# Kernel tuning notes

Measured on AMD Instinct MI355X. Metric: run time of the kernel, lower is better.

Reference implementation:

```python
import jax, jax.numpy as jnp
import numpy as np

BATCH, N_GRAPHS, N_NODES, UNITS = 512, 3, 4096, 256

def setup_inputs() -> dict:
    key = jax.random.key(0)
    ks = jax.random.split(key, 11)
    return {
        "inputs": jax.random.normal(ks[0], (BATCH, N_NODES), jnp.float32),
        "state": jax.random.normal(ks[1], (BATCH, UNITS), jnp.float32),
        "adj": jax.random.uniform(ks[2], (N_GRAPHS, N_NODES, N_NODES), jnp.float32),
        "wa": jax.random.uniform(ks[3], (N_GRAPHS,), jnp.float32),
        "w_gcn": jax.random.normal(ks[4], (N_NODES, UNITS), jnp.float32) * (1.0 / np.sqrt(N_NODES)),
        "wz": jax.random.normal(ks[5], (UNITS, UNITS), jnp.float32) * 0.05,
        "uz": jax.random.normal(ks[6], (UNITS, UNITS), jnp.float32) * 0.05,
        "bz": jax.random.normal(ks[7], (UNITS,), jnp.float32) * 0.05,
        "wh": jax.random.normal(ks[8], (UNITS, UNITS), jnp.float32) * 0.05,
        "uh": jax.random.normal(ks[9], (UNITS, UNITS), jnp.float32) * 0.05,
        "bh": jax.random.normal(ks[10], (UNITS,), jnp.float32) * 0.05,
    }

def reference(inputs, state, adj, wa, w_gcn, wz, uz, bz, wh, uh, bh):
    # Weighted sum of the n_graphs adjacency matrices: [g],[g,n,n] -> [n,n]
    adj_mix = jnp.einsum('g,gnm->nm', wa, adj)
    # Graph conv: (inputs @ adj_mix) @ w_gcn, then ReLU -> [batch, units]
    x = jax.nn.relu(jnp.matmul(jnp.matmul(inputs, adj_mix), w_gcn))
    # GRU-style gating
    z = jax.nn.sigmoid(x @ wz + state @ uz + bz)
    h_tilde = jnp.tanh(x @ wh + state @ uh + bh)
    out = (1.0 - z) * state + z * h_tilde
    return out
```

## Files before the change

kernel.cpp:

```cpp
#include <hip/hip_runtime.h>
#include <stdint.h>

typedef _Float16 f16;
typedef __attribute__((ext_vector_type(8))) _Float16 f16x8;
typedef __attribute__((ext_vector_type(4))) float f32x4;

#define NN 4096
#define UN 256

__device__ __forceinline__ f16x8 ld_f16x8(const f16* p){ return *(const f16x8*)p; }
__device__ __forceinline__ f32x4 zero4(){ f32x4 z = {0.f,0.f,0.f,0.f}; return z; }


__global__ __launch_bounds__(256) void k0_prep(
    const float* __restrict__ wg, const float* __restrict__ wz,
    const float* __restrict__ uz, const float* __restrict__ wh,
    const float* __restrict__ uh,
    f16* __restrict__ wgB,
    f16* __restrict__ czB_h, f16* __restrict__ czB_l,
    f16* __restrict__ chB_h, f16* __restrict__ chB_l)
{
  __shared__ float lsA[32*256];
  __shared__ float lsB[32*256];
  const int t = threadIdx.x;
  const int b = blockIdx.x;
  if (b < 128){
    const int kcg = b;
    #pragma unroll 8
    for (int i = 0; i < 32; i++)
      lsA[i*256 + t] = wg[(size_t)(kcg*32 + i) * UN + t];
    __syncthreads();
    #pragma unroll
    for (int i = 0; i < 4; i++){
      int o = i*256 + t;
      int l = o & 63;
      int n = ((o >> 6) << 4) + (l & 15);
      int kl = (l >> 4) * 8;
      f16 v8[8];
      #pragma unroll
      for (int j = 0; j < 8; j++) v8[j] = (f16)lsA[(kl + j)*256 + n];
      *(uint4*)(wgB + ((size_t)kcg*1024 + o)*8) = *(const uint4*)v8;
    }
  } else {
    const int kcg = b - 128;
    #pragma unroll 8
    for (int i = 0; i < 32; i++){
      int kg = kcg*32 + i;
      lsA[i*256 + t] = (kg < 256) ? wz[(size_t)kg * UN + t]
                                  : uz[(size_t)(kg - 256) * UN + t];
      lsB[i*256 + t] = (kg < 256) ? wh[(size_t)kg * UN + t]
                                  : uh[(size_t)(kg - 256) * UN + t];
    }
    __syncthreads();
    #pragma unroll
    for (int i = 0; i < 4; i++){
      int o = i*256 + t;
      int l = o & 63;
      int n = ((o >> 6) << 4) + (l & 15);
      int kl = (l >> 4) * 8;
      f16 zh[8], zl[8], hh[8], hl[8];
      #pragma unroll
      for (int j = 0; j < 8; j++){
        float vz = lsA[(kl + j)*256 + n];
        float vh = lsB[(kl + j)*256 + n];
        f16 a = (f16)vz; zh[j] = a; zl[j] = (f16)(vz - (float)a);
        f16 c = (f16)vh; hh[j] = c; hl[j] = (f16)(vh - (float)c);
      }
      size_t off = ((size_t)kcg*1024 + o)*8;
      *(uint4*)(czB_h + off) = *(const uint4*)zh;
      *(uint4*)(czB_l + off) = *(const uint4*)zl;
      *(uint4*)(chB_h + off) = *(const uint4*)hh;
      *(uint4*)(chB_l + off) = *(const uint4*)hl;
    }
  }
}

__global__ __launch_bounds__(256) void k1_w2(
    const float* __restrict__ adj, const float* __restrict__ wa,
    const f16* __restrict__ wgB, float* __restrict__ W2p)
{
  const int t = threadIdx.x, lane = t & 63, wv = t >> 6;
  const int qm = lane & 15, quad = lane >> 4;
  const int mbase = blockIdx.x * 64 + wv * 16;
  const int kbase = blockIdx.y * 512;
  const float wa0 = wa[0], wa1 = wa[1], wa2 = wa[2];
  const size_t gs = (size_t)NN * NN;
  const float* pa = adj + (size_t)(mbase + qm) * NN + kbase + quad * 8;

  f32x4 acc[16];
  #pragma unroll
  for (int i = 0; i < 16; i++) acc[i] = zero4();

  f32x4 g[6];
  #pragma unroll
  for (int r = 0; r < 2; r++)
    #pragma unroll
    for (int gi = 0; gi < 3; gi++)
      g[gi*2 + r] = *(const f32x4*)(pa + (size_t)gi*gs + r*4);

  for (int step = 0; step < 16; step++){
    const int kc = step * 32;
    const int kcg = (kbase + kc) >> 5;
    const f16* pb = wgB + ((size_t)kcg*1024 + lane)*8;

    f16x8 bf[8];
    #pragma unroll
    for (int i = 0; i < 8; i++) bf[i] = ld_f16x8(pb + i*512);

    f16x8 ah, al;
    #pragma unroll
    for (int j = 0; j < 4; j++){
      float v0 = wa0*g[0][j] + wa1*g[2][j] + wa2*g[4][j];
      float v1 = wa0*g[1][j] + wa1*g[3][j] + wa2*g[5][j];
      f16 h0 = (f16)v0, h1 = (f16)v1;
      ah[j] = h0;   al[j] = (f16)(v0 - (float)h0);
      ah[4+j] = h1; al[4+j] = (f16)(v1 - (float)h1);
    }

    f32x4 gn[6];
    if (step < 15){
      const float* pan = pa + kc + 32;
      #pragma unroll
      for (int r = 0; r < 2; r++)
        #pragma unroll
        for (int gi = 0; gi < 3; gi++)
          gn[gi*2 + r] = *(const f32x4*)(pan + (size_t)gi*gs + r*4);
    }

    f16x8 bg[8];
    #pragma unroll
    for (int i = 0; i < 8; i++) bg[i] = ld_f16x8(pb + (8+i)*512);

    #pragma unroll
    for (int tn = 0; tn < 8; tn++){
      acc[tn] = __builtin_amdgcn_mfma_f32_16x16x32_f16(ah, bf[tn], acc[tn], 0, 0, 0);
      acc[tn] = __builtin_amdgcn_mfma_f32_16x16x32_f16(al, bf[tn], acc[tn], 0, 0, 0);
    }
    #pragma unroll
    for (int tn = 0; tn < 8; tn++){
      acc[8+tn] = __builtin_amdgcn_mfma_f32_16x16x32_f16(ah, bg[tn], acc[8+tn], 0, 0, 0);
      acc[8+tn] = __builtin_amdgcn_mfma_f32_16x16x32_f16(al, bg[tn], acc[8+tn], 0, 0, 0);
    }

    #pragma unroll
    for (int i = 0; i < 6; i++) g[i] = gn[i];
  }

  float* wout = W2p + (size_t)blockIdx.y * ((size_t)NN * UN);
  #pragma unroll
  for (int tn = 0; tn < 16; tn++)
    #pragma unroll
    for (int r = 0; r < 4; r++)
      wout[(size_t)(mbase + quad*4 + r)*UN + tn*16 + qm] = acc[tn][r];
}

__global__ __launch_bounds__(256) void k_cvt(
    const float* __restrict__ W2p, f16* __restrict__ W2B)
{
  __shared__ float ls[32*256];
  const int t = threadIdx.x;
  const int kcg = blockIdx.x;
  const int r0 = t >> 6;
  const int c0 = (t & 63) * 4;
  #pragma unroll
  for (int i = 0; i < 8; i++){
    int r = i*4 + r0;
    const float* src = W2p + (size_t)(kcg*32 + r) * UN + c0;
    f32x4 s = zero4();
    #pragma unroll
    for (int p = 0; p < 8; p++)
      s = s + *(const f32x4*)(src + (size_t)p * ((size_t)NN*UN));
    *(f32x4*)(ls + r*256 + c0) = s;
  }
  __syncthreads();
  #pragma unroll
  for (int i = 0; i < 4; i++){
    int o = i*256 + t;
    int l = o & 63;
    int n = ((o >> 6) << 4) + (l & 15);
    int kl = (l >> 4) * 8;
    f16 v8[8];
    #pragma unroll
    for (int j = 0; j < 8; j++) v8[j] = (f16)ls[(kl + j)*256 + n];
    *(uint4*)(W2B + ((size_t)kcg*1024 + o)*8) = *(const uint4*)v8;
  }
}

__global__ __launch_bounds__(256) void k2_x(
    const float* __restrict__ inputs, const f16* __restrict__ W2B,
    float* __restrict__ xgp)
{
  const int t = threadIdx.x, lane = t & 63, wv = t >> 6;
  const int qm = lane & 15, quad = lane >> 4;
  const int m0 = blockIdx.x * 16;
  const int kbase = blockIdx.y * 512;
  const float* pa = inputs + (size_t)(m0 + qm) * NN + kbase + quad * 8;

  f32x4 acc[4] = { zero4(), zero4(), zero4(), zero4() };

  #pragma unroll 4
  for (int kc = 0; kc < 512; kc += 32){
    f32x4 a0 = *(const f32x4*)(pa + kc);
    f32x4 a1 = *(const f32x4*)(pa + kc + 4);
    const int kcg = (kbase + kc) >> 5;
    const f16* pb = W2B + (((size_t)kcg*16 + wv*4)*64 + lane)*8;
    f16x8 bfr[4];
    #pragma unroll
    for (int tn = 0; tn < 4; tn++) bfr[tn] = ld_f16x8(pb + tn*512);
    f16x8 ah, al;
    #pragma unroll
    for (int j = 0; j < 4; j++){
      f16 h0 = (f16)a0[j], h1 = (f16)a1[j];
      ah[j] = h0;   al[j] = (f16)(a0[j] - (float)h0);
      ah[4+j] = h1; al[4+j] = (f16)(a1[j] - (float)h1);
    }
    #pragma unroll
    for (int tn = 0; tn < 4; tn++){
      acc[tn] = __builtin_amdgcn_mfma_f32_16x16x32_f16(ah, bfr[tn], acc[tn], 0, 0, 0);
      acc[tn] = __builtin_amdgcn_mfma_f32_16x16x32_f16(al, bfr[tn], acc[tn], 0, 0, 0);
    }
  }
  float* xo = xgp + (size_t)blockIdx.y * ((size_t)512 * UN);
  #pragma unroll
  for (int tn = 0; tn < 4; tn++)
    #pragma unroll
    for (int r = 0; r < 4; r++)
      xo[(size_t)(m0 + quad*4 + r)*UN + (wv*4 + tn)*16 + qm] = acc[tn][r];
}

__global__ __launch_bounds__(256) void k2b_xa(
    const float* __restrict__ xgp, const float* __restrict__ state,
    f16* __restrict__ xa_h, f16* __restrict__ xa_l)
{
  const size_t e = ((size_t)blockIdx.x * 256 + threadIdx.x) * 8;
  const int m = (int)(e >> 9), k0 = (int)(e & 511);
  const bool rl = (k0 < 256);
  f32x4 a, b;
  if (rl){
    const float* src = xgp + (size_t)m * UN + k0;
    a = zero4(); b = zero4();
    #pragma unroll
    for (int p = 0; p < 8; p++){
      a = a + *(const f32x4*)(src + (size_t)p * (512*UN));
      b = b + *(const f32x4*)(src + (size_t)p * (512*UN) + 4);
    }
  } else {
    const float* src = state + (size_t)m * UN + (k0 - 256);
    a = *(const f32x4*)src;
    b = *(const f32x4*)(src + 4);
  }
  f16 hi[8], lo[8];
  #pragma unroll
  for (int j = 0; j < 4; j++){
    float va = rl ? fmaxf(a[j], 0.f) : a[j];
    float vb = rl ? fmaxf(b[j], 0.f) : b[j];
    f16 ha = (f16)va, hb = (f16)vb;
    hi[j] = ha;   lo[j] = (f16)(va - (float)ha);
    hi[4+j] = hb; lo[4+j] = (f16)(vb - (float)hb);
  }
  *(uint4*)(xa_h + e) = *(const uint4*)hi;
  *(uint4*)(xa_l + e) = *(const uint4*)lo;
}

__global__ __launch_bounds__(256) void k3_gates(
    const f16* __restrict__ xa_h, const f16* __restrict__ xa_l,
    const f16* __restrict__ czB_h, const f16* __restrict__ czB_l,
    const f16* __restrict__ chB_h, const f16* __restrict__ chB_l,
    float* __restrict__ lzp, float* __restrict__ lhp)
{
  const int t = threadIdx.x, lane = t & 63, wv = t >> 6;
  const int qm = lane & 15, quad = lane >> 4;
  const int m0 = blockIdx.x * 16;
  const int kbase = blockIdx.y * 64;

  f32x4 az[4] = { zero4(), zero4(), zero4(), zero4() };
  f32x4 ag[4] = { zero4(), zero4(), zero4(), zero4() };

  #pragma unroll
  for (int kk = 0; kk < 2; kk++){
    const int kb = kbase + kk*32;
    const size_t pao = (size_t)(m0 + qm) * 512 + kb + quad * 8;
    f16x8 ah = ld_f16x8(xa_h + pao);
    f16x8 al = ld_f16x8(xa_l + pao);
    const int kcg = kb >> 5;
    const size_t base = (((size_t)kcg*16 + wv*4)*64 + lane)*8;
    #pragma unroll
    for (int tn = 0; tn < 4; tn++){
      f16x8 bzh = ld_f16x8(czB_h + base + tn*512);
      f16x8 bzl = ld_f16x8(czB_l + base + tn*512);
      f16x8 bhh = ld_f16x8(chB_h + base + tn*512);
      f16x8 bhl = ld_f16x8(chB_l + base + tn*512);
      az[tn] = __builtin_amdgcn_mfma_f32_16x16x32_f16(ah, bzh, az[tn], 0, 0, 0);
      az[tn] = __builtin_amdgcn_mfma_f32_16x16x32_f16(al, bzh, az[tn], 0, 0, 0);
      az[tn] = __builtin_amdgcn_mfma_f32_16x16x32_f16(ah, bzl, az[tn], 0, 0, 0);
      ag[tn] = __builtin_amdgcn_mfma_f32_16x16x32_f16(ah, bhh, ag[tn], 0, 0, 0);
      ag[tn] = __builtin_amdgcn_mfma_f32_16x16x32_f16(al, bhh, ag[tn], 0, 0, 0);
      ag[tn] = __builtin_amdgcn_mfma_f32_16x16x32_f16(ah, bhl, ag[tn], 0, 0, 0);
    }
  }
  float* oz = lzp + (size_t)blockIdx.y * ((size_t)512 * UN);
  float* oh = lhp + (size_t)blockIdx.y * ((size_t)512 * UN);
  #pragma unroll
  for (int tn = 0; tn < 4; tn++)
    #pragma unroll
    for (int r = 0; r < 4; r++){
      size_t o = (size_t)(m0 + quad*4 + r)*UN + (wv*4 + tn)*16 + qm;
      oz[o] = az[tn][r];
      oh[o] = ag[tn][r];
    }
}

__global__ __launch_bounds__(256) void k3b_out(
    const float* __restrict__ lzp, const float* __restrict__ lhp,
    const float* __restrict__ state,
    const float* __restrict__ bz, const float* __restrict__ bh,
    float* __restrict__ out)
{
  const size_t e = ((size_t)blockIdx.x * 256 + threadIdx.x) * 4;
  const int n = (int)(e & 255);
  f32x4 z4 = zero4(), h4 = zero4();
  #pragma unroll
  for (int p = 0; p < 8; p++){
    z4 = z4 + *(const f32x4*)(lzp + (size_t)p * (512*UN) + e);
    h4 = h4 + *(const f32x4*)(lhp + (size_t)p * (512*UN) + e);
  }
  f32x4 s4 = *(const f32x4*)(state + e);
  f32x4 bz4 = *(const f32x4*)(bz + n);
  f32x4 bh4 = *(const f32x4*)(bh + n);
  f32x4 o4;
  #pragma unroll
  for (int j = 0; j < 4; j++){
    float z = 1.f / (1.f + __expf(-(z4[j] + bz4[j])));
    float ex = __expf(2.f * (h4[j] + bh4[j]));
    float hh = 1.f - 2.f / (ex + 1.f);
    o4[j] = (1.f - z) * s4[j] + z * hh;
  }
  *(f32x4*)(out + e) = o4;
}

extern "C" void kernel_launch(void* const* d_in, const int* in_sizes, int n_in,
                              void* d_out, int out_size, void* d_ws, size_t ws_size,
                              hipStream_t stream)
{
  const float* inputs = (const float*)d_in[0];
  const float* state  = (const float*)d_in[1];
  const float* adj    = (const float*)d_in[2];
  const float* wa     = (const float*)d_in[3];
  const float* wg     = (const float*)d_in[4];
  const float* wz     = (const float*)d_in[5];
  const float* uz     = (const float*)d_in[6];
  const float* bz     = (const float*)d_in[7];
  const float* wh     = (const float*)d_in[8];
  const float* uh     = (const float*)d_in[9];
  const float* bh     = (const float*)d_in[10];
  float* out = (float*)d_out;

  char* ws = (char*)d_ws;
  float* W2p   = (float*)(ws);
  float* xgp   = (float*)(ws + (32u<<20));
  float* lzp   = (float*)(ws + (36u<<20));
  float* lhp   = (float*)(ws + (40u<<20));
  f16* wgB     = (f16*)(ws + (44u<<20));
  f16* W2B     = (f16*)(ws + (46u<<20));
  f16* xa_h    = (f16*)(ws + (48u<<20));
  f16* xa_l    = (f16*)(ws + (48u<<20) + (512u<<10));
  f16* czB_h   = (f16*)(ws + (49u<<20));
  f16* czB_l   = (f16*)(ws + (49u<<20) + (256u<<10));
  f16* chB_h   = (f16*)(ws + (49u<<20) + (512u<<10));
  f16* chB_l   = (f16*)(ws + (49u<<20) + (768u<<10));

  k0_prep<<<144, 256, 0, stream>>>(wg, wz, uz, wh, uh,
                                   wgB, czB_h, czB_l, chB_h, chB_l);
  k1_w2<<<dim3(64, 8), 256, 0, stream>>>(adj, wa, wgB, W2p);
  k_cvt<<<128, 256, 0, stream>>>(W2p, W2B);
  k2_x<<<dim3(32, 8), 256, 0, stream>>>(inputs, W2B, xgp);
  k2b_xa<<<128, 256, 0, stream>>>(xgp, state, xa_h, xa_l);
  k3_gates<<<dim3(32, 8), 256, 0, stream>>>(xa_h, xa_l, czB_h, czB_l,
                                            chB_h, chB_l, lzp, lhp);
  k3b_out<<<128, 256, 0, stream>>>(lzp, lhp, state, bz, bh, out);
}
```

Before: 347.9 us.

## Precompute adjacency mix in a separate pass and fuse the gate tail kernels

A new streaming kernel forms the weighted adjacency sum once and writes it as hi/lo f16 planes. The W2 GEMM then loads ready-made f16 fragments instead of reading three fp32 adjacency tensors and mixing them in-loop. The xa prep, gate GEMM and output epilogue are merged into one 32-block kernel that stages activations in shared memory, which removes the split-K partial buffers and two launches. The cost is an extra 64 MB write and read of the f16 planes, plus a tail kernel with only 32 blocks and a serial K loop.

After: 417.9 us. +20.1%, slower.

```diff
diff --git a/kernel.cpp b/kernel.cpp
--- a/kernel.cpp
+++ b/kernel.cpp
@@ -11,6 +11,29 @@
 __device__ __forceinline__ f16x8 ld_f16x8(const f16* p){ return *(const f16x8*)p; }
 __device__ __forceinline__ f32x4 zero4(){ f32x4 z = {0.f,0.f,0.f,0.f}; return z; }
 
+
+__global__ __launch_bounds__(256) void kmix(
+    const float* __restrict__ adj, const float* __restrict__ wa,
+    f16* __restrict__ mixh, f16* __restrict__ mixl)
+{
+  const float wa0 = wa[0], wa1 = wa[1], wa2 = wa[2];
+  const size_t gs = (size_t)NN * NN;
+  const size_t stride = (size_t)gridDim.x * 256 * 4;
+  for (size_t i = ((size_t)blockIdx.x * 256 + threadIdx.x) * 4; i < gs; i += stride){
+    f32x4 a0 = *(const f32x4*)(adj + i);
+    f32x4 a1 = *(const f32x4*)(adj + gs + i);
+    f32x4 a2 = *(const f32x4*)(adj + 2*gs + i);
+    f16 h4[4], l4[4];
+    #pragma unroll
+    for (int j = 0; j < 4; j++){
+      float v = wa0*a0[j] + wa1*a1[j] + wa2*a2[j];
+      f16 hh = (f16)v;
+      h4[j] = hh; l4[j] = (f16)(v - (float)hh);
+    }
+    *(uint2*)(mixh + i) = *(const uint2*)h4;
+    *(uint2*)(mixl + i) = *(const uint2*)l4;
+  }
+}
 
 __global__ __launch_bounds__(256) void k0_prep(
     const float* __restrict__ wg, const float* __restrict__ wz,
@@ -76,27 +99,23 @@
 }
 
 __global__ __launch_bounds__(256) void k1_w2(
-    const float* __restrict__ adj, const float* __restrict__ wa,
+    const f16* __restrict__ mixh, const f16* __restrict__ mixl,
     const f16* __restrict__ wgB, float* __restrict__ W2p)
 {
   const int t = threadIdx.x, lane = t & 63, wv = t >> 6;
   const int qm = lane & 15, quad = lane >> 4;
   const int mbase = blockIdx.x * 64 + wv * 16;
   const int kbase = blockIdx.y * 512;
-  const float wa0 = wa[0], wa1 = wa[1], wa2 = wa[2];
-  const size_t gs = (size_t)NN * NN;
-  const float* pa = adj + (size_t)(mbase + qm) * NN + kbase + quad * 8;
+  const size_t arow = (size_t)(mbase + qm) * NN + kbase + quad * 8;
+  const f16* pah = mixh + arow;
+  const f16* pal = mixl + arow;
 
   f32x4 acc[16];
   #pragma unroll
   for (int i = 0; i < 16; i++) acc[i] = zero4();
 
-  f32x4 g[6];
-  #pragma unroll
-  for (int r = 0; r < 2; r++)
-    #pragma unroll
-    for (int gi = 0; gi < 3; gi++)
-      g[gi*2 + r] = *(const f32x4*)(pa + (size_t)gi*gs + r*4);
+  f16x8 ah = ld_f16x8(pah);
+  f16x8 al = ld_f16x8(pal);
 
   for (int step = 0; step < 16; step++){
     const int kc = step * 32;
@@ -106,30 +125,15 @@
     f16x8 bf[8];
     #pragma unroll
     for (int i = 0; i < 8; i++) bf[i] = ld_f16x8(pb + i*512);
-
-    f16x8 ah, al;
-    #pragma unroll
-    for (int j = 0; j < 4; j++){
-      float v0 = wa0*g[0][j] + wa1*g[2][j] + wa2*g[4][j];
-      float v1 = wa0*g[1][j] + wa1*g[3][j] + wa2*g[5][j];
-      f16 h0 = (f16)v0, h1 = (f16)v1;
-      ah[j] = h0;   al[j] = (f16)(v0 - (float)h0);
-      ah[4+j] = h1; al[4+j] = (f16)(v1 - (float)h1);
-    }
-
-    f32x4 gn[6];
+    f16x8 bg[8];
+    #pragma unroll
+    for (int i = 0; i < 8; i++) bg[i] = ld_f16x8(pb + (8+i)*512);
+
+    f16x8 ahn = ah, aln = al;
     if (step < 15){
-      const float* pan = pa + kc + 32;
-      #pragma unroll
-      for (int r = 0; r < 2; r++)
-        #pragma unroll
-        for (int gi = 0; gi < 3; gi++)
-          gn[gi*2 + r] = *(const f32x4*)(pan + (size_t)gi*gs + r*4);
-    }
-
-    f16x8 bg[8];
-    #pragma unroll
-    for (int i = 0; i < 8; i++) bg[i] = ld_f16x8(pb + (8+i)*512);
+      ahn = ld_f16x8(pah + kc + 32);
+      aln = ld_f16x8(pal + kc + 32);
+    }
 
     #pragma unroll
     for (int tn = 0; tn < 8; tn++){
@@ -142,8 +146,7 @@
       acc[8+tn] = __builtin_amdgcn_mfma_f32_16x16x32_f16(al, bg[tn], acc[8+tn], 0, 0, 0);
     }
 
-    #pragma unroll
-    for (int i = 0; i < 6; i++) g[i] = gn[i];
+    ah = ahn; al = aln;
   }
 
   float* wout = W2p + (size_t)blockIdx.y * ((size_t)NN * UN);
@@ -228,60 +231,55 @@
       xo[(size_t)(m0 + quad*4 + r)*UN + (wv*4 + tn)*16 + qm] = acc[tn][r];
 }
 
-__global__ __launch_bounds__(256) void k2b_xa(
+__global__ __launch_bounds__(256) void k_tail(
     const float* __restrict__ xgp, const float* __restrict__ state,
-    f16* __restrict__ xa_h, f16* __restrict__ xa_l)
-{
-  const size_t e = ((size_t)blockIdx.x * 256 + threadIdx.x) * 8;
-  const int m = (int)(e >> 9), k0 = (int)(e & 511);
-  const bool rl = (k0 < 256);
-  f32x4 a, b;
-  if (rl){
-    const float* src = xgp + (size_t)m * UN + k0;
-    a = zero4(); b = zero4();
-    #pragma unroll
-    for (int p = 0; p < 8; p++){
-      a = a + *(const f32x4*)(src + (size_t)p * (512*UN));
-      b = b + *(const f32x4*)(src + (size_t)p * (512*UN) + 4);
-    }
-  } else {
-    const float* src = state + (size_t)m * UN + (k0 - 256);
-    a = *(const f32x4*)src;
-    b = *(const f32x4*)(src + 4);
-  }
-  f16 hi[8], lo[8];
-  #pragma unroll
-  for (int j = 0; j < 4; j++){
-    float va = rl ? fmaxf(a[j], 0.f) : a[j];
-    float vb = rl ? fmaxf(b[j], 0.f) : b[j];
-    f16 ha = (f16)va, hb = (f16)vb;
-    hi[j] = ha;   lo[j] = (f16)(va - (float)ha);
-    hi[4+j] = hb; lo[4+j] = (f16)(vb - (float)hb);
-  }
-  *(uint4*)(xa_h + e) = *(const uint4*)hi;
-  *(uint4*)(xa_l + e) = *(const uint4*)lo;
-}
-
-__global__ __launch_bounds__(256) void k3_gates(
-    const f16* __restrict__ xa_h, const f16* __restrict__ xa_l,
     const f16* __restrict__ czB_h, const f16* __restrict__ czB_l,
     const f16* __restrict__ chB_h, const f16* __restrict__ chB_l,
-    float* __restrict__ lzp, float* __restrict__ lhp)
-{
-  const int t = threadIdx.x, lane = t & 63, wv = t >> 6;
+    const float* __restrict__ bz, const float* __restrict__ bh,
+    float* __restrict__ out)
+{
+  __shared__ f16 xah[16][520];
+  __shared__ f16 xal[16][520];
+  const int t = threadIdx.x;
+  const int m0 = blockIdx.x * 16;
+
+  {
+    const int r = t >> 4, cb = (t & 15) * 16;
+    #pragma unroll
+    for (int cc = 0; cc < 16; cc += 4){
+      const int c = cb + cc;
+      const float* src = xgp + (size_t)(m0 + r) * UN + c;
+      f32x4 s = zero4();
+      #pragma unroll
+      for (int p = 0; p < 8; p++)
+        s = s + *(const f32x4*)(src + (size_t)p * (512*UN));
+      f16 h4[4], l4[4];
+      #pragma unroll
+      for (int j = 0; j < 4; j++){
+        float v = fmaxf(s[j], 0.f);
+        f16 hh = (f16)v; h4[j] = hh; l4[j] = (f16)(v - (float)hh);
+      }
+      *(uint2*)&xah[r][c] = *(const uint2*)h4;
+      *(uint2*)&xal[r][c] = *(const uint2*)l4;
+      f32x4 st = *(const f32x4*)(state + (size_t)(m0 + r) * UN + c);
+      #pragma unroll
+      for (int j = 0; j < 4; j++){
+        f16 hh = (f16)st[j]; h4[j] = hh; l4[j] = (f16)(st[j] - (float)hh);
+      }
+      *(uint2*)&xah[r][256 + c] = *(const uint2*)h4;
+      *(uint2*)&xal[r][256 + c] = *(const uint2*)l4;
+    }
+  }
+  __syncthreads();
+
+  const int lane = t & 63, wv = t >> 6;
   const int qm = lane & 15, quad = lane >> 4;
-  const int m0 = blockIdx.x * 16;
-  const int kbase = blockIdx.y * 64;
-
   f32x4 az[4] = { zero4(), zero4(), zero4(), zero4() };
   f32x4 ag[4] = { zero4(), zero4(), zero4(), zero4() };
 
-  #pragma unroll
-  for (int kk = 0; kk < 2; kk++){
-    const int kb = kbase + kk*32;
-    const size_t pao = (size_t)(m0 + qm) * 512 + kb + quad * 8;
-    f16x8 ah = ld_f16x8(xa_h + pao);
-    f16x8 al = ld_f16x8(xa_l + pao);
+  for (int kb = 0; kb < 512; kb += 32){
+    f16x8 ah = *(const f16x8*)&xah[qm][kb + quad*8];
+    f16x8 al = *(const f16x8*)&xal[qm][kb + quad*8];
     const int kcg = kb >> 5;
     const size_t base = (((size_t)kcg*16 + wv*4)*64 + lane)*8;
     #pragma unroll
@@ -298,44 +296,21 @@
       ag[tn] = __builtin_amdgcn_mfma_f32_16x16x32_f16(ah, bhl, ag[tn], 0, 0, 0);
     }
   }
-  float* oz = lzp + (size_t)blockIdx.y * ((size_t)512 * UN);
-  float* oh = lhp + (size_t)blockIdx.y * ((size_t)512 * UN);
-  #pragma unroll
-  for (int tn = 0; tn < 4; tn++)
+
+  #pragma unroll
+  for (int tn = 0; tn < 4; tn++){
+    const int col = (wv*4 + tn)*16 + qm;
+    const float bzv = bz[col], bhv = bh[col];
     #pragma unroll
     for (int r = 0; r < 4; r++){
-      size_t o = (size_t)(m0 + quad*4 + r)*UN + (wv*4 + tn)*16 + qm;
-      oz[o] = az[tn][r];
-      oh[o] = ag[tn][r];
-    }
-}
-
-__global__ __launch_bounds__(256) void k3b_out(
-    const float* __restrict__ lzp, const float* __restrict__ lhp,
-    const float* __restrict__ state,
-    const float* __restrict__ bz, const float* __restrict__ bh,
-    float* __restrict__ out)
-{
-  const size_t e = ((size_t)blockIdx.x * 256 + threadIdx.x) * 4;
-  const int n = (int)(e & 255);
-  f32x4 z4 = zero4(), h4 = zero4();
-  #pragma unroll
-  for (int p = 0; p < 8; p++){
-    z4 = z4 + *(const f32x4*)(lzp + (size_t)p * (512*UN) + e);
-    h4 = h4 + *(const f32x4*)(lhp + (size_t)p * (512*UN) + e);
-  }
-  f32x4 s4 = *(const f32x4*)(state + e);
-  f32x4 bz4 = *(const f32x4*)(bz + n);
-  f32x4 bh4 = *(const f32x4*)(bh + n);
-  f32x4 o4;
-  #pragma unroll
-  for (int j = 0; j < 4; j++){
-    float z = 1.f / (1.f + __expf(-(z4[j] + bz4[j])));
-    float ex = __expf(2.f * (h4[j] + bh4[j]));
-    float hh = 1.f - 2.f / (ex + 1.f);
-    o4[j] = (1.f - z) * s4[j] + z * hh;
-  }
-  *(f32x4*)(out + e) = o4;
+      const int row = m0 + quad*4 + r;
+      const float s = state[(size_t)row*UN + col];
+      float z = 1.f / (1.f + __expf(-(az[tn][r] + bzv)));
+      float ex = __expf(2.f * (ag[tn][r] + bhv));
+      float hh = 1.f - 2.f / (ex + 1.f);
+      out[(size_t)row*UN + col] = (1.f - z) * s + z * hh;
+    }
+  }
 }
 
 extern "C" void kernel_launch(void* const* d_in, const int* in_sizes, int n_in,
@@ -356,26 +331,23 @@
   float* out = (float*)d_out;
 
   char* ws = (char*)d_ws;
-  float* W2p   = (float*)(ws);
-  float* xgp   = (float*)(ws + (32u<<20));
-  float* lzp   = (float*)(ws + (36u<<20));
-  float* lhp   = (float*)(ws + (40u<<20));
-  f16* wgB     = (f16*)(ws + (44u<<20));
-  f16* W2B     = (f16*)(ws + (46u<<20));
-  f16* xa_h    = (f16*)(ws + (48u<<20));
-  f16* xa_l    = (f16*)(ws + (48u<<20) + (512u<<10));
-  f16* czB_h   = (f16*)(ws + (49u<<20));
-  f16* czB_l   = (f16*)(ws + (49u<<20) + (256u<<10));
-  f16* chB_h   = (f16*)(ws + (49u<<20) + (512u<<10));
-  f16* chB_l   = (f16*)(ws + (49u<<20) + (768u<<10));
-
+  f16* mixh    = (f16*)(ws);
+  f16* mixl    = (f16*)(ws + (32u<<20));
+  float* W2p   = (float*)(ws + (64u<<20));
+  float* xgp   = (float*)(ws + (96u<<20));
+  f16* wgB     = (f16*)(ws + (100u<<20));
+  f16* W2B     = (f16*)(ws + (102u<<20));
+  f16* czB_h   = (f16*)(ws + (104u<<20));
+  f16* czB_l   = (f16*)(ws + (104u<<20) + (256u<<10));
+  f16* chB_h   = (f16*)(ws + (104u<<20) + (512u<<10));
+  f16* chB_l   = (f16*)(ws + (104u<<20) + (768u<<10));
+
+  kmix<<<2048, 256, 0, stream>>>(adj, wa, mixh, mixl);
   k0_prep<<<144, 256, 0, stream>>>(wg, wz, uz, wh, uh,
                                    wgB, czB_h, czB_l, chB_h, chB_l);
-  k1_w2<<<dim3(64, 8), 256, 0, stream>>>(adj, wa, wgB, W2p);
+  k1_w2<<<dim3(64, 8), 256, 0, stream>>>(mixh, mixl, wgB, W2p);
   k_cvt<<<128, 256, 0, stream>>>(W2p, W2B);
   k2_x<<<dim3(32, 8), 256, 0, stream>>>(inputs, W2B, xgp);
-  k2b_xa<<<128, 256, 0, stream>>>(xgp, state, xa_h, xa_l);
-  k3_gates<<<dim3(32, 8), 256, 0, stream>>>(xa_h, xa_l, czB_h, czB_l,
-                                            chB_h, chB_l, lzp, lhp);
-  k3b_out<<<128, 256, 0, stream>>>(lzp, lhp, state, bz, bh, out);
-}
+  k_tail<<<32, 256, 0, stream>>>(xgp, state, czB_h, czB_l, chB_h, chB_l,
+                                 bz, bh, out);
+}
```
